# Optimization experiments

Hardware: AMD Instinct MI355X
Metric: run time of the kernel (lower is better)

## Reference

```python
import jax, jax.numpy as jnp
import numpy as np


def setup_inputs() -> dict:
    key = jax.random.key(0)
    x = jax.random.normal(key, (8192, 24576), dtype=jnp.float32)
    return {"x": x, "k": 64}


def reference(x, k):
    # top-k along last dim, keep only those entries, zero the rest
    _, idx = jax.lax.top_k(x, k)                      # idx: [N, k]
    rows = jnp.arange(x.shape[0])[:, None]            # [N, 1]
    mask = jnp.zeros(x.shape, dtype=bool).at[rows, idx].set(True)
    return x * mask
```

## Files before the change

kernel.cpp:

```cpp
#include <hip/hip_runtime.h>
#include <stdint.h>

#define NCOLS 24576
#define BLOCK 256
#define CAP   2048
#define T0KEY 0xC0000000u

__device__ __forceinline__ uint32_t f2k(float f) {
    uint32_t u = __float_as_uint(f);
    return (u & 0x80000000u) ? ~u : (u | 0x80000000u);
}
__device__ __forceinline__ float k2f(uint32_t k) {
    uint32_t u = (k & 0x80000000u) ? (k ^ 0x80000000u) : ~k;
    return __uint_as_float(u);
}

__global__ __launch_bounds__(BLOCK, 4)
void topk_filter_kernel(const float* __restrict__ in, const int* __restrict__ kp,
                        float* __restrict__ out, int nrows) {
    __shared__ uint64_t cand[CAP];
    __shared__ int hist[256];
    __shared__ int s_cnt;
    __shared__ int s_bin, s_rem;

    const int row = blockIdx.x;
    if (row >= nrows) return;
    const int tid  = threadIdx.x;
    const int lane = tid & 63;
    const int k    = *kp;

    const float4* inr  = (const float4*)(in  + (size_t)row * NCOLS);
    float4*       outr = (float4*)(out + (size_t)row * NCOLS);
    float*        outrow = out + (size_t)row * NCOLS;
    const float*  inrow  = in  + (size_t)row * NCOLS;

    if (tid == 0) s_cnt = 0;
    __syncthreads();

    const float4 z4 = make_float4(0.f, 0.f, 0.f, 0.f);
    #pragma unroll 4
    for (int i = 0; i < NCOLS / (BLOCK * 4); ++i) {
        int v4 = i * BLOCK + tid;
        float4 v = inr[v4];
        outr[v4] = z4;
        uint32_t keys[4] = {f2k(v.x), f2k(v.y), f2k(v.z), f2k(v.w)};
        #pragma unroll
        for (int j = 0; j < 4; ++j) {
            bool pred = keys[j] >= T0KEY;
            unsigned long long m = __ballot(pred);
            if (m) {
                int cnt = __popcll(m);
                int leader = __ffsll(m) - 1;
                int pos = 0;
                if (lane == leader) pos = atomicAdd(&s_cnt, cnt);
                pos = __shfl(pos, leader);
                if (pred) {
                    int my = pos + __popcll(m & ((1ull << lane) - 1ull));
                    if (my < CAP) {
                        uint32_t c = (uint32_t)(v4 * 4 + j);
                        cand[my] = ((uint64_t)keys[j] << 32) | (0xFFFFFFFFu - c);
                    }
                }
            }
        }
    }
    __syncthreads();
    const int n_total = s_cnt;
    const bool fast = (n_total <= CAP) && (n_total >= k) && (k > 0);

    if (fast) {
        const int n = n_total;
        uint32_t prefix = 0; int rem = k;
        for (int shift = 24; shift >= 0; shift -= 8) {
            for (int b = tid; b < 256; b += BLOCK) hist[b] = 0;
            __syncthreads();
            for (int i = tid; i < n; i += BLOCK) {
                uint32_t key = (uint32_t)(cand[i] >> 32);
                uint32_t hi = (uint32_t)shift + 8u;
                bool match = (hi >= 32u) || ((key >> hi) == (prefix >> hi));
                if (match) atomicAdd(&hist[(key >> shift) & 0xFF], 1);
            }
            __syncthreads();
            if (tid == 0) {
                int cum = 0, b = 255;
                for (; b > 0; --b) { cum += hist[b]; if (cum >= rem) break; }
                if (cum < rem) cum += hist[0];
                s_bin = b; s_rem = rem - (cum - hist[b]);
            }
            __syncthreads();
            prefix |= ((uint32_t)s_bin) << shift;
            rem = s_rem;
            __syncthreads();
        }
        const uint32_t T = prefix;
        const int r = rem;

        for (int i = tid; i < n; i += BLOCK) {
            uint64_t p = cand[i];
            uint32_t key = (uint32_t)(p >> 32);
            bool keep = false;
            if (key > T) keep = true;
            else if (key == T) {
                int rank = 0;
                for (int j = 0; j < n; ++j) {
                    uint64_t q = cand[j];
                    if ((uint32_t)(q >> 32) == T && q > p) rank++;
                }
                keep = (rank < r);
            }
            if (keep) {
                uint32_t c = 0xFFFFFFFFu - (uint32_t)p;
                outrow[c] = k2f(key);
            }
        }
    } else {
        int kk = k;
        if (kk <= 0) return;
        if (kk > NCOLS) kk = NCOLS;
        uint32_t prefix = 0; int rem = kk;
        for (int shift = 24; shift >= 0; shift -= 8) {
            for (int b = tid; b < 256; b += BLOCK) hist[b] = 0;
            __syncthreads();
            for (int i = tid; i < NCOLS; i += BLOCK) {
                uint32_t key = f2k(inrow[i]);
                uint32_t hi = (uint32_t)shift + 8u;
                bool match = (hi >= 32u) || ((key >> hi) == (prefix >> hi));
                if (match) atomicAdd(&hist[(key >> shift) & 0xFF], 1);
            }
            __syncthreads();
            if (tid == 0) {
                int cum = 0, b = 255;
                for (; b > 0; --b) { cum += hist[b]; if (cum >= rem) break; }
                if (cum < rem) cum += hist[0];
                s_bin = b; s_rem = rem - (cum - hist[b]);
            }
            __syncthreads();
            prefix |= ((uint32_t)s_bin) << shift;
            rem = s_rem;
            __syncthreads();
        }
        const uint32_t T = prefix;
        const int r = rem;
        if (tid < 64) {
            int running = 0;
            for (int base = 0; base < NCOLS; base += 64) {
                int c = base + tid;
                float x = inrow[c];
                uint32_t key = f2k(x);
                bool eq = (key == T);
                unsigned long long m = __ballot(eq);
                if (key > T) outrow[c] = x;
                else if (eq) {
                    int rank = running + __popcll(m & ((1ull << tid) - 1ull));
                    if (rank < r) outrow[c] = x;
                }
                running += __popcll(m);
            }
        }
    }
}

extern "C" void kernel_launch(void* const* d_in, const int* in_sizes, int n_in,
                              void* d_out, int out_size, void* d_ws, size_t ws_size,
                              hipStream_t stream) {
    const float* x  = (const float*)d_in[0];
    const int*   kp = (const int*)d_in[1];
    float*       o  = (float*)d_out;
    const int nrows = in_sizes[0] / NCOLS;
    topk_filter_kernel<<<nrows, BLOCK, 0, stream>>>(x, kp, o, nrows);
}
```

Before: 1.411 ms.

## Batch row loads, use per-thread candidate atomics, and parallelize histogram bin search

The streaming pass now issues eight float4 loads and eight zero stores per thread at once before compacting, which raises memory-level parallelism. Candidate compaction drops the wave ballot/shuffle in favour of one LDS atomicAdd per thread per float4 that has any candidates. The serial single-thread scan over 256 histogram bins is replaced by a 64-lane suffix scan using shuffles. Candidates are sparse, so the change in atomics matters less, but the extra register pressure from the 8-deep batch could lower occupancy.

```diff
diff --git a/kernel.cpp b/kernel.cpp
--- a/kernel.cpp
+++ b/kernel.cpp
@@ -25,9 +25,8 @@
 
     const int row = blockIdx.x;
     if (row >= nrows) return;
-    const int tid  = threadIdx.x;
-    const int lane = tid & 63;
-    const int k    = *kp;
+    const int tid = threadIdx.x;
+    const int k   = *kp;
 
     const float4* inr  = (const float4*)(in  + (size_t)row * NCOLS);
     float4*       outr = (float4*)(out + (size_t)row * NCOLS);
@@ -38,29 +37,23 @@
     __syncthreads();
 
     const float4 z4 = make_float4(0.f, 0.f, 0.f, 0.f);
-    #pragma unroll 4
-    for (int i = 0; i < NCOLS / (BLOCK * 4); ++i) {
-        int v4 = i * BLOCK + tid;
-        float4 v = inr[v4];
-        outr[v4] = z4;
-        uint32_t keys[4] = {f2k(v.x), f2k(v.y), f2k(v.z), f2k(v.w)};
+    for (int m = 0; m < 3; ++m) {
+        float4 v[8];
         #pragma unroll
-        for (int j = 0; j < 4; ++j) {
-            bool pred = keys[j] >= T0KEY;
-            unsigned long long m = __ballot(pred);
-            if (m) {
-                int cnt = __popcll(m);
-                int leader = __ffsll(m) - 1;
-                int pos = 0;
-                if (lane == leader) pos = atomicAdd(&s_cnt, cnt);
-                pos = __shfl(pos, leader);
-                if (pred) {
-                    int my = pos + __popcll(m & ((1ull << lane) - 1ull));
-                    if (my < CAP) {
-                        uint32_t c = (uint32_t)(v4 * 4 + j);
-                        cand[my] = ((uint64_t)keys[j] << 32) | (0xFFFFFFFFu - c);
-                    }
-                }
+        for (int j = 0; j < 8; ++j) v[j] = inr[(m * 8 + j) * BLOCK + tid];
+        #pragma unroll
+        for (int j = 0; j < 8; ++j) outr[(m * 8 + j) * BLOCK + tid] = z4;
+        #pragma unroll
+        for (int j = 0; j < 8; ++j) {
+            uint32_t k0 = f2k(v[j].x), k1 = f2k(v[j].y), k2 = f2k(v[j].z), k3 = f2k(v[j].w);
+            int c = (k0 >= T0KEY) + (k1 >= T0KEY) + (k2 >= T0KEY) + (k3 >= T0KEY);
+            if (c) {
+                int pos = atomicAdd(&s_cnt, c);
+                uint32_t base = (uint32_t)(((m * 8 + j) * BLOCK + tid) * 4);
+                if (k0 >= T0KEY) { if (pos < CAP) cand[pos] = ((uint64_t)k0 << 32) | (0xFFFFFFFFu - base);       pos++; }
+                if (k1 >= T0KEY) { if (pos < CAP) cand[pos] = ((uint64_t)k1 << 32) | (0xFFFFFFFFu - (base + 1)); pos++; }
+                if (k2 >= T0KEY) { if (pos < CAP) cand[pos] = ((uint64_t)k2 << 32) | (0xFFFFFFFFu - (base + 2)); pos++; }
+                if (k3 >= T0KEY) { if (pos < CAP) cand[pos] = ((uint64_t)k3 << 32) | (0xFFFFFFFFu - (base + 3)); pos++; }
             }
         }
     }
@@ -72,20 +65,34 @@
         const int n = n_total;
         uint32_t prefix = 0; int rem = k;
         for (int shift = 24; shift >= 0; shift -= 8) {
-            for (int b = tid; b < 256; b += BLOCK) hist[b] = 0;
+            hist[tid] = 0;
             __syncthreads();
+            const uint32_t hi = (uint32_t)shift + 8u;
             for (int i = tid; i < n; i += BLOCK) {
                 uint32_t key = (uint32_t)(cand[i] >> 32);
-                uint32_t hi = (uint32_t)shift + 8u;
                 bool match = (hi >= 32u) || ((key >> hi) == (prefix >> hi));
                 if (match) atomicAdd(&hist[(key >> shift) & 0xFF], 1);
             }
             __syncthreads();
-            if (tid == 0) {
-                int cum = 0, b = 255;
-                for (; b > 0; --b) { cum += hist[b]; if (cum >= rem) break; }
-                if (cum < rem) cum += hist[0];
-                s_bin = b; s_rem = rem - (cum - hist[b]);
+            if (tid < 64) {
+                int h0 = hist[tid * 4], h1 = hist[tid * 4 + 1],
+                    h2 = hist[tid * 4 + 2], h3 = hist[tid * 4 + 3];
+                int tot = h0 + h1 + h2 + h3;
+                int t = tot;
+                #pragma unroll
+                for (int off = 1; off < 64; off <<= 1) {
+                    int u = __shfl_down(t, off);
+                    if (tid + off < 64) t += u;
+                }
+                int above = t - tot;
+                int S3 = h3 + above;
+                int S2 = h2 + S3;
+                int S1 = h1 + S2;
+                int S0 = h0 + S1;
+                if (S0 >= rem && S0 - h0 < rem) { s_bin = tid * 4 + 0; s_rem = rem - (S0 - h0); }
+                if (S1 >= rem && S1 - h1 < rem) { s_bin = tid * 4 + 1; s_rem = rem - (S1 - h1); }
+                if (S2 >= rem && S2 - h2 < rem) { s_bin = tid * 4 + 2; s_rem = rem - (S2 - h2); }
+                if (S3 >= rem && S3 - h3 < rem) { s_bin = tid * 4 + 3; s_rem = rem - (S3 - h3); }
             }
             __syncthreads();
             prefix |= ((uint32_t)s_bin) << shift;
@@ -119,11 +126,11 @@
         if (kk > NCOLS) kk = NCOLS;
         uint32_t prefix = 0; int rem = kk;
         for (int shift = 24; shift >= 0; shift -= 8) {
-            for (int b = tid; b < 256; b += BLOCK) hist[b] = 0;
+            hist[tid] = 0;
             __syncthreads();
+            const uint32_t hi = (uint32_t)shift + 8u;
             for (int i = tid; i < NCOLS; i += BLOCK) {
                 uint32_t key = f2k(inrow[i]);
-                uint32_t hi = (uint32_t)shift + 8u;
                 bool match = (hi >= 32u) || ((key >> hi) == (prefix >> hi));
                 if (match) atomicAdd(&hist[(key >> shift) & 0xFF], 1);
             }
@@ -148,13 +155,13 @@
                 float x = inrow[c];
                 uint32_t key = f2k(x);
                 bool eq = (key == T);
-                unsigned long long m = __ballot(eq);
+                unsigned long long mm = __ballot(eq);
                 if (key > T) outrow[c] = x;
                 else if (eq) {
-                    int rank = running + __popcll(m & ((1ull << tid) - 1ull));
+                    int rank = running + __popcll(mm & ((1ull << tid) - 1ull));
                     if (rank < r) outrow[c] = x;
                 }
-                running += __popcll(m);
+                running += __popcll(mm);
             }
         }
     }
```

Result: faster. 1.318 ms (-6.6%).
